# Optimization experiments

Measured on AMD Instinct MI355X. Metric: run time of the kernel, lower is better.

## Reference

```python
import jax, jax.numpy as jnp
import numpy as np

F_MIN = 0.8  # f_min from init

def setup_inputs() -> dict:
    key = jax.random.key(0)
    k0, k1, k2, k3, k4 = jax.random.split(key, 5)
    b, t, h, d = 4, 2048, 16, 128
    q = jax.random.normal(k0, (b, t, h, d), dtype=jnp.float32)
    k = jax.random.normal(k1, (b, t, h, d), dtype=jnp.float32)
    v = jax.random.normal(k2, (b, t, h, d), dtype=jnp.float32)
    f_gate = jax.random.uniform(k3, (b, t, h, d), dtype=jnp.float32)
    g_gate = jax.random.uniform(k4, (b, t, h, d), dtype=jnp.float32)
    return {"q": q, "k": k, "v": v, "f_gate": f_gate, "g_gate": g_gate}

def reference(q, k, v, f_gate, g_gate):
    # Gated delta-rule recurrence (DeltaRuleGated.forward, attn_mask=None):
    #   M_t = M_{t-1} * clip(f_t outer f_t, f_min, 1) + (k_t*g_t) outer (v_t*g_t)
    #   o_t = q_t @ M_t
    b, t, h, d = q.shape

    def step(M, xs):
        qi, ki, vi, fi, gi = xs  # each [b, h, d]
        f_outer = jnp.clip(fi[..., :, None] * fi[..., None, :], F_MIN, 1.0)  # [b,h,d,d]
        kg = ki * gi
        vg = vi * gi
        M = M * f_outer + kg[..., :, None] * vg[..., None, :]
        oi = jnp.einsum('bhd,bhde->bhe', qi, M)
        return M, oi

    xs = tuple(jnp.moveaxis(a, 1, 0) for a in (q, k, v, f_gate, g_gate))  # [t,b,h,d]
    M0 = jnp.zeros((b, h, d, d), dtype=q.dtype)
    _, out = jax.lax.scan(step, M0, xs)  # out: [t, b, h, d]
    return jnp.moveaxis(out, 0, 1)  # [b, t, h, d]
```

## Files before the change

kernel.cpp:

```cpp
#include <hip/hip_runtime.h>

#define T_DIM 2048
#define H_DIM 16
#define D_DIM 128
#define TC 32
#define NCG 4
#define CPB 32

typedef float v2f __attribute__((ext_vector_type(2)));

__device__ __forceinline__ float blo(unsigned u){ return __uint_as_float(u << 16); }
__device__ __forceinline__ float bhi(unsigned u){ return __uint_as_float(u & 0xffff0000u); }
__device__ __forceinline__ unsigned f2bf(float x){
  unsigned u = __float_as_uint(x);
  return (u + 0x7fffu + ((u >> 16) & 1u)) >> 16;
}
__device__ __forceinline__ uint2 pack4(float4 v){
  uint2 r;
  r.x = f2bf(v.x) | (f2bf(v.y) << 16);
  r.y = f2bf(v.z) | (f2bf(v.w) << 16);
  return r;
}
__device__ __forceinline__ v2f up2(unsigned u){
  v2f r; r.x = __uint_as_float(u << 16); r.y = __uint_as_float(u & 0xffff0000u); return r;
}
#if defined(__has_builtin) && __has_builtin(__builtin_elementwise_fma)
__device__ __forceinline__ v2f v2fma(v2f a, v2f b, v2f c){ return __builtin_elementwise_fma(a, b, c); }
#else
__device__ __forceinline__ v2f v2fma(v2f a, v2f b, v2f c){ v2f r; r.x=fmaf(a.x,b.x,c.x); r.y=fmaf(a.y,b.y,c.y); return r; }
#endif
__device__ __forceinline__ float row_sum16(float x){
  x += __int_as_float(__builtin_amdgcn_update_dpp(0, __float_as_int(x), 0x121, 0xf, 0xf, true));
  x += __int_as_float(__builtin_amdgcn_update_dpp(0, __float_as_int(x), 0x122, 0xf, 0xf, true));
  x += __int_as_float(__builtin_amdgcn_update_dpp(0, __float_as_int(x), 0x124, 0xf, 0xf, true));
  x += __int_as_float(__builtin_amdgcn_update_dpp(0, __float_as_int(x), 0x128, 0xf, 0xf, true));
  return x;
}

__global__ __launch_bounds__(256, 1)
void deltanet_kernel(const float* __restrict__ qg,
                     const float* __restrict__ kg,
                     const float* __restrict__ vg,
                     const float* __restrict__ fg,
                     const float* __restrict__ gg,
                     float* __restrict__ out)
{
  __shared__ unsigned short qs [TC][D_DIM];
  __shared__ unsigned short fs [TC][D_DIM];
  __shared__ unsigned short kgs[TC][D_DIM];
  __shared__ unsigned short vgs[TC][D_DIM];
  __shared__ float obuf[TC][CPB];

  const int tid  = threadIdx.x;
  const int blk  = blockIdx.x;
  const int pair = blk >> 2;
  const int cg   = blk & 3;
  const int bb   = pair >> 4;
  const int hh   = pair & 15;
  const int cc   = tid >> 4;
  const int rc   = tid & 15;
  const int c0   = cg * CPB + cc * 2;
  const int r0   = rc * 8;

  const size_t base0 = ((size_t)bb * T_DIM * H_DIM + hh) * (size_t)D_DIM;
  const float* qp = qg + base0;
  const float* kp = kg + base0;
  const float* vp = vg + base0;
  const float* fp = fg + base0;
  const float* gp = gg + base0;
  float*       op = out + base0;

  v2f M0[4], M1[4];
  #pragma unroll
  for (int j = 0; j < 4; ++j) { M0[j] = (v2f){0.f,0.f}; M1[j] = (v2f){0.f,0.f}; }

  for (int t0 = 0; t0 < T_DIM; t0 += TC) {
    #pragma unroll
    for (int it = 0; it < 4; ++it) {
      const int flat = (it * 256 + tid) * 4;
      const int s = flat >> 7;
      const int r = flat & 127;
      const size_t go = (size_t)(t0 + s) * (H_DIM * D_DIM) + r;
      float4 qv = *(const float4*)(qp + go);
      float4 fv = *(const float4*)(fp + go);
      *(uint2*)&qs[s][r] = pack4(qv);
      *(uint2*)&fs[s][r] = pack4(fv);
      float4 kv = *(const float4*)(kp + go);
      float4 gv = *(const float4*)(gp + go);
      float4 vv = *(const float4*)(vp + go);
      float4 kgv = make_float4(kv.x*gv.x, kv.y*gv.y, kv.z*gv.z, kv.w*gv.w);
      float4 vgv = make_float4(vv.x*gv.x, vv.y*gv.y, vv.z*gv.z, vv.w*gv.w);
      *(uint2*)&kgs[s][r] = pack4(kgv);
      *(uint2*)&vgs[s][r] = pack4(vgv);
    }
    __syncthreads();

    uint4 q4 = *(const uint4*)&qs [0][r0];
    uint4 f4 = *(const uint4*)&fs [0][r0];
    uint4 k4 = *(const uint4*)&kgs[0][r0];
    unsigned fcp = *(const unsigned*)&fs [0][c0];
    unsigned vcp = *(const unsigned*)&vgs[0][c0];

    #pragma unroll 4
    for (int s = 0; s < TC; ++s) {
      const uint4 q4c = q4, f4c = f4, k4c = k4;
      const unsigned fcpc = fcp, vcpc = vcp;
      if (s + 1 < TC) {
        q4  = *(const uint4*)&qs [s+1][r0];
        f4  = *(const uint4*)&fs [s+1][r0];
        k4  = *(const uint4*)&kgs[s+1][r0];
        fcp = *(const unsigned*)&fs [s+1][c0];
        vcp = *(const unsigned*)&vgs[s+1][c0];
      }
      const float fc0 = blo(fcpc), fc1 = bhi(fcpc);
      const float vc0 = blo(vcpc), vc1 = bhi(vcpc);
      const v2f fcv0 = (v2f){fc0, fc0}, fcv1 = (v2f){fc1, fc1};
      const v2f vcv0 = (v2f){vc0, vc0}, vcv1 = (v2f){vc1, vc1};
      const unsigned* qa = (const unsigned*)&q4c;
      const unsigned* fa = (const unsigned*)&f4c;
      const unsigned* kk = (const unsigned*)&k4c;
      v2f po0 = (v2f){0.f,0.f}, po1 = (v2f){0.f,0.f};
      #pragma unroll
      for (int j = 0; j < 4; ++j) {
        const v2f qr = up2(qa[j]);
        const v2f fr = up2(fa[j]);
        const v2f kr = up2(kk[j]);
        v2f t0 = fr * fcv0;
        v2f t1 = fr * fcv1;
        t0.x = fmaxf(t0.x, 0.8f); t0.y = fmaxf(t0.y, 0.8f);
        t1.x = fmaxf(t1.x, 0.8f); t1.y = fmaxf(t1.y, 0.8f);
        M0[j] = v2fma(M0[j], t0, kr * vcv0);
        M1[j] = v2fma(M1[j], t1, kr * vcv1);
        po0 = v2fma(qr, M0[j], po0);
        po1 = v2fma(qr, M1[j], po1);
      }
      float p0 = po0.x + po0.y;
      float p1 = po1.x + po1.y;
      p0 = row_sum16(p0);
      p1 = row_sum16(p1);
      if (rc == 0) {
        obuf[s][cc*2]   = p0;
        obuf[s][cc*2+1] = p1;
      }
    }
    __syncthreads();

    {
      const int s = tid >> 3;
      const int c = (tid & 7) * 4;
      float4 ov = *(const float4*)&obuf[s][c];
      *(float4*)(op + (size_t)(t0 + s) * (H_DIM * D_DIM) + cg * CPB + c) = ov;
    }
  }
}

extern "C" void kernel_launch(void* const* d_in, const int* in_sizes, int n_in,
                              void* d_out, int out_size, void* d_ws, size_t ws_size,
                              hipStream_t stream) {
  const float* q = (const float*)d_in[0];
  const float* k = (const float*)d_in[1];
  const float* v = (const float*)d_in[2];
  const float* f = (const float*)d_in[3];
  const float* g = (const float*)d_in[4];
  float* out = (float*)d_out;
  deltanet_kernel<<<dim3(64 * NCG), dim3(256), 0, stream>>>(q, k, v, f, g, out);
}
```

Before: 830.5 us.

## Double threads per block, prefetch next chunk into registers, keep f/kg in fp32

Each block now uses 512 threads, each holding a 4x2 slice of the state instead of 8x2, so the per-step row reduction is split across two half-waves and combined through a doubled output buffer. Global loads for the next time chunk are issued into registers right after the barrier so they overlap with the recurrence compute. The f and k*g tiles are stored in LDS as fp32 instead of bf16, and the column f/v values are interleaved into one small array so a single float4 read fetches both. The clamp now uses a packed vector max. This adds register pressure from the prefetch buffers and more LDS traffic in exchange for shorter per-thread serial chains and hidden load latency.

```diff
diff --git a/kernel.cpp b/kernel.cpp
--- a/kernel.cpp
+++ b/kernel.cpp
@@ -9,8 +9,6 @@
 
 typedef float v2f __attribute__((ext_vector_type(2)));
 
-__device__ __forceinline__ float blo(unsigned u){ return __uint_as_float(u << 16); }
-__device__ __forceinline__ float bhi(unsigned u){ return __uint_as_float(u & 0xffff0000u); }
 __device__ __forceinline__ unsigned f2bf(float x){
   unsigned u = __float_as_uint(x);
   return (u + 0x7fffu + ((u >> 16) & 1u)) >> 16;
@@ -28,6 +26,11 @@
 __device__ __forceinline__ v2f v2fma(v2f a, v2f b, v2f c){ return __builtin_elementwise_fma(a, b, c); }
 #else
 __device__ __forceinline__ v2f v2fma(v2f a, v2f b, v2f c){ v2f r; r.x=fmaf(a.x,b.x,c.x); r.y=fmaf(a.y,b.y,c.y); return r; }
+#endif
+#if defined(__has_builtin) && __has_builtin(__builtin_elementwise_max)
+__device__ __forceinline__ v2f v2max(v2f a, v2f b){ return __builtin_elementwise_max(a, b); }
+#else
+__device__ __forceinline__ v2f v2max(v2f a, v2f b){ v2f r; r.x=fmaxf(a.x,b.x); r.y=fmaxf(a.y,b.y); return r; }
 #endif
 __device__ __forceinline__ float row_sum16(float x){
   x += __int_as_float(__builtin_amdgcn_update_dpp(0, __float_as_int(x), 0x121, 0xf, 0xf, true));
@@ -37,7 +40,7 @@
   return x;
 }
 
-__global__ __launch_bounds__(256, 1)
+__global__ __launch_bounds__(512, 2)
 void deltanet_kernel(const float* __restrict__ qg,
                      const float* __restrict__ kg,
                      const float* __restrict__ vg,
@@ -45,11 +48,11 @@
                      const float* __restrict__ gg,
                      float* __restrict__ out)
 {
-  __shared__ unsigned short qs [TC][D_DIM];
-  __shared__ unsigned short fs [TC][D_DIM];
-  __shared__ unsigned short kgs[TC][D_DIM];
-  __shared__ unsigned short vgs[TC][D_DIM];
-  __shared__ float obuf[TC][CPB];
+  __shared__ unsigned short qs[TC][D_DIM];
+  __shared__ __align__(16) float fs [TC][D_DIM];
+  __shared__ __align__(16) float kgs[TC][D_DIM];
+  __shared__ __align__(16) float cols[TC][2*CPB];
+  __shared__ float obuf[2][TC][CPB];
 
   const int tid  = threadIdx.x;
   const int blk  = blockIdx.x;
@@ -57,10 +60,10 @@
   const int cg   = blk & 3;
   const int bb   = pair >> 4;
   const int hh   = pair & 15;
-  const int cc   = tid >> 4;
-  const int rc   = tid & 15;
-  const int c0   = cg * CPB + cc * 2;
-  const int r0   = rc * 8;
+  const int rc   = tid & 31;
+  const int cc   = tid >> 5;
+  const int r0   = rc * 4;
+  const int lc0  = cc * 2;
 
   const size_t base0 = ((size_t)bb * T_DIM * H_DIM + hh) * (size_t)D_DIM;
   const float* qp = qg + base0;
@@ -70,86 +73,116 @@
   const float* gp = gg + base0;
   float*       op = out + base0;
 
-  v2f M0[4], M1[4];
+  v2f M0[2], M1[2];
   #pragma unroll
-  for (int j = 0; j < 4; ++j) { M0[j] = (v2f){0.f,0.f}; M1[j] = (v2f){0.f,0.f}; }
+  for (int j = 0; j < 2; ++j) { M0[j] = (v2f){0.f,0.f}; M1[j] = (v2f){0.f,0.f}; }
+
+  const int fl0 = tid * 4;
+  const int s0g = fl0 >> 7, r0g = fl0 & 127;
+  const int fl1 = (512 + tid) * 4;
+  const int s1g = fl1 >> 7, r1g = fl1 & 127;
+  const bool cv0 = ((r0g >> 5) == cg);
+  const bool cv1 = ((r1g >> 5) == cg);
+
+  float4 rq[2], rf[2], rk[2], rg[2], rv[2];
+
+  {
+    const size_t go0 = (size_t)s0g * (H_DIM * D_DIM) + r0g;
+    const size_t go1 = (size_t)s1g * (H_DIM * D_DIM) + r1g;
+    rq[0] = *(const float4*)(qp + go0); rq[1] = *(const float4*)(qp + go1);
+    rf[0] = *(const float4*)(fp + go0); rf[1] = *(const float4*)(fp + go1);
+    rk[0] = *(const float4*)(kp + go0); rk[1] = *(const float4*)(kp + go1);
+    rg[0] = *(const float4*)(gp + go0); rg[1] = *(const float4*)(gp + go1);
+    if (cv0) rv[0] = *(const float4*)(vp + go0);
+    if (cv1) rv[1] = *(const float4*)(vp + go1);
+  }
 
   for (int t0 = 0; t0 < T_DIM; t0 += TC) {
     #pragma unroll
-    for (int it = 0; it < 4; ++it) {
-      const int flat = (it * 256 + tid) * 4;
-      const int s = flat >> 7;
-      const int r = flat & 127;
-      const size_t go = (size_t)(t0 + s) * (H_DIM * D_DIM) + r;
-      float4 qv = *(const float4*)(qp + go);
-      float4 fv = *(const float4*)(fp + go);
-      *(uint2*)&qs[s][r] = pack4(qv);
-      *(uint2*)&fs[s][r] = pack4(fv);
-      float4 kv = *(const float4*)(kp + go);
-      float4 gv = *(const float4*)(gp + go);
-      float4 vv = *(const float4*)(vp + go);
-      float4 kgv = make_float4(kv.x*gv.x, kv.y*gv.y, kv.z*gv.z, kv.w*gv.w);
-      float4 vgv = make_float4(vv.x*gv.x, vv.y*gv.y, vv.z*gv.z, vv.w*gv.w);
-      *(uint2*)&kgs[s][r] = pack4(kgv);
-      *(uint2*)&vgs[s][r] = pack4(vgv);
+    for (int it = 0; it < 2; ++it) {
+      const int s = it ? s1g : s0g;
+      const int r = it ? r1g : r0g;
+      const float4 q4 = rq[it], f4 = rf[it], k4 = rk[it], g4 = rg[it];
+      *(uint2*)&qs[s][r]   = pack4(q4);
+      *(float4*)&fs[s][r]  = f4;
+      *(float4*)&kgs[s][r] = (float4){k4.x*g4.x, k4.y*g4.y, k4.z*g4.z, k4.w*g4.w};
+      if (it ? cv1 : cv0) {
+        const float4 v4 = rv[it];
+        const int c2 = (r & 31) * 2;
+        *(float4*)&cols[s][c2]     = (float4){f4.x, v4.x*g4.x, f4.y, v4.y*g4.y};
+        *(float4*)&cols[s][c2 + 4] = (float4){f4.z, v4.z*g4.z, f4.w, v4.w*g4.w};
+      }
     }
     __syncthreads();
 
-    uint4 q4 = *(const uint4*)&qs [0][r0];
-    uint4 f4 = *(const uint4*)&fs [0][r0];
-    uint4 k4 = *(const uint4*)&kgs[0][r0];
-    unsigned fcp = *(const unsigned*)&fs [0][c0];
-    unsigned vcp = *(const unsigned*)&vgs[0][c0];
+    if (t0 + TC < T_DIM) {
+      const size_t go0 = (size_t)(t0 + TC + s0g) * (H_DIM * D_DIM) + r0g;
+      const size_t go1 = (size_t)(t0 + TC + s1g) * (H_DIM * D_DIM) + r1g;
+      rq[0] = *(const float4*)(qp + go0); rq[1] = *(const float4*)(qp + go1);
+      rf[0] = *(const float4*)(fp + go0); rf[1] = *(const float4*)(fp + go1);
+      rk[0] = *(const float4*)(kp + go0); rk[1] = *(const float4*)(kp + go1);
+      rg[0] = *(const float4*)(gp + go0); rg[1] = *(const float4*)(gp + go1);
+      if (cv0) rv[0] = *(const float4*)(vp + go0);
+      if (cv1) rv[1] = *(const float4*)(vp + go1);
+    }
+
+    uint2  q2  = *(const uint2*)&qs[0][r0];
+    float4 f4r = *(const float4*)&fs[0][r0];
+    float4 k4r = *(const float4*)&kgs[0][r0];
+    float4 cbv = *(const float4*)&cols[0][2*lc0];
 
     #pragma unroll 4
     for (int s = 0; s < TC; ++s) {
-      const uint4 q4c = q4, f4c = f4, k4c = k4;
-      const unsigned fcpc = fcp, vcpc = vcp;
+      const uint2  q2c = q2;
+      const float4 f4c = f4r, k4c = k4r, cbc = cbv;
       if (s + 1 < TC) {
-        q4  = *(const uint4*)&qs [s+1][r0];
-        f4  = *(const uint4*)&fs [s+1][r0];
-        k4  = *(const uint4*)&kgs[s+1][r0];
-        fcp = *(const unsigned*)&fs [s+1][c0];
-        vcp = *(const unsigned*)&vgs[s+1][c0];
-      }
-      const float fc0 = blo(fcpc), fc1 = bhi(fcpc);
-      const float vc0 = blo(vcpc), vc1 = bhi(vcpc);
-      const v2f fcv0 = (v2f){fc0, fc0}, fcv1 = (v2f){fc1, fc1};
-      const v2f vcv0 = (v2f){vc0, vc0}, vcv1 = (v2f){vc1, vc1};
-      const unsigned* qa = (const unsigned*)&q4c;
-      const unsigned* fa = (const unsigned*)&f4c;
-      const unsigned* kk = (const unsigned*)&k4c;
+        q2  = *(const uint2*)&qs[s+1][r0];
+        f4r = *(const float4*)&fs[s+1][r0];
+        k4r = *(const float4*)&kgs[s+1][r0];
+        cbv = *(const float4*)&cols[s+1][2*lc0];
+      }
+      const v2f fcv0 = (v2f){cbc.x, cbc.x};
+      const v2f vcv0 = (v2f){cbc.y, cbc.y};
+      const v2f fcv1 = (v2f){cbc.z, cbc.z};
+      const v2f vcv1 = (v2f){cbc.w, cbc.w};
+      const v2f c08  = (v2f){0.8f, 0.8f};
       v2f po0 = (v2f){0.f,0.f}, po1 = (v2f){0.f,0.f};
-      #pragma unroll
-      for (int j = 0; j < 4; ++j) {
-        const v2f qr = up2(qa[j]);
-        const v2f fr = up2(fa[j]);
-        const v2f kr = up2(kk[j]);
-        v2f t0 = fr * fcv0;
-        v2f t1 = fr * fcv1;
-        t0.x = fmaxf(t0.x, 0.8f); t0.y = fmaxf(t0.y, 0.8f);
-        t1.x = fmaxf(t1.x, 0.8f); t1.y = fmaxf(t1.y, 0.8f);
-        M0[j] = v2fma(M0[j], t0, kr * vcv0);
-        M1[j] = v2fma(M1[j], t1, kr * vcv1);
-        po0 = v2fma(qr, M0[j], po0);
-        po1 = v2fma(qr, M1[j], po1);
+      {
+        const v2f fr = (v2f){f4c.x, f4c.y};
+        const v2f kr = (v2f){k4c.x, k4c.y};
+        const v2f qr = up2(q2c.x);
+        M0[0] = v2fma(M0[0], v2max(fr * fcv0, c08), kr * vcv0);
+        M1[0] = v2fma(M1[0], v2max(fr * fcv1, c08), kr * vcv1);
+        po0 = v2fma(qr, M0[0], po0);
+        po1 = v2fma(qr, M1[0], po1);
+      }
+      {
+        const v2f fr = (v2f){f4c.z, f4c.w};
+        const v2f kr = (v2f){k4c.z, k4c.w};
+        const v2f qr = up2(q2c.y);
+        M0[1] = v2fma(M0[1], v2max(fr * fcv0, c08), kr * vcv0);
+        M1[1] = v2fma(M1[1], v2max(fr * fcv1, c08), kr * vcv1);
+        po0 = v2fma(qr, M0[1], po0);
+        po1 = v2fma(qr, M1[1], po1);
       }
       float p0 = po0.x + po0.y;
       float p1 = po1.x + po1.y;
       p0 = row_sum16(p0);
       p1 = row_sum16(p1);
-      if (rc == 0) {
-        obuf[s][cc*2]   = p0;
-        obuf[s][cc*2+1] = p1;
+      if ((rc & 15) == 0) {
+        *(v2f*)&obuf[rc >> 4][s][lc0] = (v2f){p0, p1};
       }
     }
     __syncthreads();
 
     {
-      const int s = tid >> 3;
-      const int c = (tid & 7) * 4;
-      float4 ov = *(const float4*)&obuf[s][c];
-      *(float4*)(op + (size_t)(t0 + s) * (H_DIM * D_DIM) + cg * CPB + c) = ov;
+      const int flat = tid * 2;
+      const int s = flat >> 5;
+      const int c = flat & 31;
+      const v2f a = *(const v2f*)&obuf[0][s][c];
+      const v2f b = *(const v2f*)&obuf[1][s][c];
+      const v2f o = a + b;
+      *(v2f*)(op + (size_t)(t0 + s) * (H_DIM * D_DIM) + cg * CPB + c) = o;
     }
   }
 }
@@ -163,5 +196,5 @@
   const float* f = (const float*)d_in[3];
   const float* g = (const float*)d_in[4];
   float* out = (float*)d_out;
-  deltanet_kernel<<<dim3(64 * NCG), dim3(256), 0, stream>>>(q, k, v, f, g, out);
-}
+  deltanet_kernel<<<dim3(64 * NCG), dim3(512), 0, stream>>>(q, k, v, f, g, out);
+}
```

Measured after the change: 692.0 us. 16.7% less time.
